# Optimization experiments

Measured on AMD Instinct MI355X. Metric: run time of the kernel, lower is better.

The kernel has to match this reference:

```python
import jax, jax.numpy as jnp
import numpy as np

N = 100000          # total nodes (ground + sub)
G = 50000           # ground nodes (first G)
E = 800000          # edges per edge set
H = 64              # hidden_features
F_IN = 32           # node_features
MAX_DEG = 20        # MFConv max_degree
NUM_GRAPHS = 128
DEPTH = 1
LN_EPS = 1e-5


def setup_inputs() -> dict:
    key = jax.random.key(0)
    ks = jax.random.split(key, 12)

    def edges(k):
        return jax.random.randint(k, (2, E), 0, N, dtype=jnp.int32)

    return {
        "x": jax.random.normal(ks[0], (N, F_IN), jnp.float32),
        "edge_index": edges(ks[1]),
        "subgraph_edge_index": edges(ks[2]),
        "node_subnode_index": edges(ks[3]),
        "subnode_node_index": edges(ks[4]),
        "ground_node": jnp.arange(N) < G,
        "subgraph_batch_index": jax.random.randint(ks[5], (N - G,), 0, NUM_GRAPHS, dtype=jnp.int32),
        "batch_idx": jax.random.randint(ks[6], (N,), 0, NUM_GRAPHS, dtype=jnp.int32),
        # learned parameters
        "emb_w": jax.random.normal(ks[7], (F_IN, H), jnp.float32) / np.sqrt(F_IN).astype(np.float32),
        "emb_b": jnp.zeros((H,), jnp.float32),
        # 4 MFConvs per depth, 21 degree buckets each; lins_l has bias, lins_r has none
        "conv_wl": jax.random.normal(ks[8], (DEPTH, 4, MAX_DEG + 1, H, H), jnp.float32) / np.sqrt(H).astype(np.float32),
        "conv_bl": jnp.zeros((DEPTH, 4, MAX_DEG + 1, H), jnp.float32),
        "conv_wr": jax.random.normal(ks[9], (DEPTH, 4, MAX_DEG + 1, H, H), jnp.float32) / np.sqrt(H).astype(np.float32),
        "ln_g": jnp.ones((DEPTH, H), jnp.float32),
        "ln_b": jnp.zeros((DEPTH, H), jnp.float32),
        "out_w": jax.random.normal(ks[10], (H, 1), jnp.float32) / np.sqrt(H).astype(np.float32),
        "out_b": jnp.zeros((1,), jnp.float32),
    }


def _mfconv(x, ei, wl, bl, wr):
    """PyG MFConv: out_i = lins_l[deg_i](sum_{j->i} x_j) + lins_r[deg_i](x_i).
    Returns (out, update_mask) where update_mask marks nodes receiving >=1 message
    (catch_lone_sender equivalent)."""
    src, dst = ei[0], ei[1]
    n = x.shape[0]
    deg = jax.ops.segment_sum(jnp.ones(src.shape, jnp.float32), dst, num_segments=n)
    d = jnp.minimum(deg.astype(jnp.int32), MAX_DEG)
    h = jax.ops.segment_sum(x[src], dst, num_segments=n)      # [N, H] neighbor sum
    out = jnp.zeros_like(x)
    for k in range(MAX_DEG + 1):                              # fixed 21 degree buckets
        m = (d == k)[:, None]
        out = out + jnp.where(m, h @ wl[k] + bl[k] + x @ wr[k], 0.0)
    return out, deg > 0


def _layernorm(h, g, b):
    mu = jnp.mean(h, axis=-1, keepdims=True)
    var = jnp.mean(jnp.square(h - mu), axis=-1, keepdims=True)
    return (h - mu) * jax.lax.rsqrt(var + LN_EPS) * g + b


def reference(x, edge_index, subgraph_edge_index, node_subnode_index,
              subnode_node_index, ground_node, subgraph_batch_index, batch_idx,
              emb_w, emb_b, conv_wl, conv_bl, conv_wr, ln_g, ln_b, out_w, out_b):
    h = x @ emb_w + emb_b                                     # embedding
    eis = (edge_index, node_subnode_index, subgraph_edge_index, subnode_node_index)
    for i in range(DEPTH):
        if i != 0:
            h = jax.nn.relu(h)
        h0 = h                                                # residual skip
        for j, ei in enumerate(eis):
            out, upd = _mfconv(h, ei, conv_wl[i, j], conv_bl[i, j], conv_wr[i, j])
            h = jnp.where(upd[:, None], out, h)               # masking=True restore
            if j < 3:
                h = jax.nn.relu(h)
        h = _layernorm(h, ln_g[i], ln_b[i])
        h = h + h0
    # global_add_pool over ground nodes only
    pooled = jax.ops.segment_sum(jnp.where(ground_node[:, None], h, 0.0),
                                 batch_idx, num_segments=NUM_GRAPHS)
    return pooled @ out_w + out_b
```

## Files before the change

### kernel.cpp

```cpp
#include <hip/hip_runtime.h>

#define N_NODES 100000
#define G_NODES 50000
#define N_EDGES 800000
#define H 64
#define F_IN 32
#define MAX_DEG 20
#define NUM_GRAPHS 128
#define LN_EPS 1e-5f
#define POOL_BLOCKS 256
#define MAX_TILES 1600

#define NBINS 512
#define BPB 782
#define CHUNK 6250
#define MKEYS (4 * N_NODES)
#define MEDGES (4 * N_EDGES)

typedef __attribute__((ext_vector_type(8))) short short8;
typedef __attribute__((ext_vector_type(4))) float float4v;

static __device__ __forceinline__ unsigned short f2b(float f) {
  unsigned u = __float_as_uint(f);
  return (unsigned short)((u + 0x7fffu + ((u >> 16) & 1u)) >> 16);
}
static __device__ __forceinline__ float b2f(unsigned short b) {
  return __uint_as_float(((unsigned)b) << 16);
}

__global__ __launch_bounds__(256) void emb_kernel(
    const float* __restrict__ x, const unsigned short* __restrict__ ewbt,
    const float* __restrict__ eb, float* __restrict__ h0,
    unsigned short* __restrict__ ab, float* __restrict__ pooled) {
  int tid = threadIdx.x;
  if (blockIdx.x == 0) {
    for (int i = tid; i < NUM_GRAPHS * H; i += 256) pooled[i] = 0.f;
  }
  int base = blockIdx.x * 64;
  int nIn = min(64, N_NODES - base);
  int qw = tid >> 6, lane = tid & 63;
  __shared__ unsigned short aL[64 * 40];
  __shared__ float outF[64 * 68];

  {
    int node = tid >> 2, chb = (tid & 3) * 8;
    unsigned short v8[8];
    if (node < nIn) {
      const float* xr = x + ((size_t)(base + node)) * F_IN + chb;
      float4 f0 = *(const float4*)(xr);
      float4 f1 = *(const float4*)(xr + 4);
      v8[0] = f2b(f0.x); v8[1] = f2b(f0.y); v8[2] = f2b(f0.z); v8[3] = f2b(f0.w);
      v8[4] = f2b(f1.x); v8[5] = f2b(f1.y); v8[6] = f2b(f1.z); v8[7] = f2b(f1.w);
    } else {
#pragma unroll
      for (int i = 0; i < 8; ++i) v8[i] = 0;
    }
    *(short8*)&aL[(tid >> 2) * 40 + chb] = *(short8*)v8;
  }

  int m = lane & 15, quad = lane >> 4;
  short8 a = *(const short8*)&aL[(qw * 16 + m) * 40 + quad * 8];
  float4v acc[4];
#pragma unroll
  for (int t = 0; t < 4; ++t) {
    float bv = eb[t * 16 + m];
    acc[t] = (float4v){bv, bv, bv, bv};
  }
#pragma unroll
  for (int t = 0; t < 4; ++t) {
    short8 bf = *(const short8*)&ewbt[(t * 16 + m) * F_IN + quad * 8];
    acc[t] = __builtin_amdgcn_mfma_f32_16x16x32_bf16(a, bf, acc[t], 0, 0, 0);
  }
#pragma unroll
  for (int t = 0; t < 4; ++t)
#pragma unroll
    for (int r = 0; r < 4; ++r)
      outF[(qw * 16 + quad * 4 + r) * 68 + t * 16 + m] = acc[t][r];
  for (int r = qw * 16; r < qw * 16 + 16; ++r) {
    if (r < nIn) {
      int node = base + r;
      float v = outF[r * 68 + lane];
      if (node < G_NODES) h0[node * H + lane] = v;
      ab[node * 128 + 64 + lane] = f2b(v);
    }
  }
}

__global__ __launch_bounds__(256) void wconv_kernel(
    const float* __restrict__ wl, const float* __restrict__ wr,
    const float* __restrict__ ew, unsigned short* __restrict__ wbt,
    unsigned short* __restrict__ ewbt) {
  int i = blockIdx.x * 256 + threadIdx.x;
  if (i < 84 * 64 * 128) {
    int k = i & 127;
    int ch = (i >> 7) & 63;
    int jb = i >> 13;
    float v = (k < 64) ? wl[jb * 4096 + k * 64 + ch]
                       : wr[jb * 4096 + (k - 64) * 64 + ch];
    wbt[i] = f2b(v);
  } else if (i < 84 * 64 * 128 + H * F_IN) {
    int ii = i - 84 * 64 * 128;
    int c = ii >> 5, f = ii & 31;
    ewbt[ii] = f2b(ew[f * H + c]);
  }
}

__global__ __launch_bounds__(256) void p1_bincount(
    const int* __restrict__ e0, const int* __restrict__ e1,
    const int* __restrict__ e2, const int* __restrict__ e3,
    int* __restrict__ cntT) {
  __shared__ int hist[NBINS];
  int t = threadIdx.x, b = blockIdx.x;
  for (int i = t; i < NBINS; i += 256) hist[i] = 0;
  __syncthreads();
  int j = b >> 7;
  const int* ei = (j == 0) ? e0 : (j == 1) ? e1 : (j == 2) ? e2 : e3;
  int ebase = (b & 127) * CHUNK;
  for (int i = t; i < CHUNK; i += 256) {
    int dst = ei[N_EDGES + ebase + i];
    int key = j * N_NODES + dst;
    atomicAdd(&hist[key / BPB], 1);
  }
  __syncthreads();
  for (int i = t; i < NBINS; i += 256) cntT[i * NBINS + b] = hist[i];
}

__global__ __launch_bounds__(256) void p3_binscatter(
    const int* __restrict__ e0, const int* __restrict__ e1,
    const int* __restrict__ e2, const int* __restrict__ e3,
    const int* __restrict__ offT, const int* __restrict__ bsumA,
    unsigned* __restrict__ binned) {
  __shared__ int cur[NBINS];
  int t = threadIdx.x, b = blockIdx.x;
  for (int i = t; i < NBINS; i += 256) {
    int idx = i * NBINS + b;
    cur[i] = offT[idx] + bsumA[idx >> 10];
  }
  __syncthreads();
  int j = b >> 7;
  const int* ei = (j == 0) ? e0 : (j == 1) ? e1 : (j == 2) ? e2 : e3;
  int ebase = (b & 127) * CHUNK;
  for (int i = t; i < CHUNK; i += 256) {
    int src = ei[ebase + i];
    int dst = ei[N_EDGES + ebase + i];
    int key = j * N_NODES + dst;
    int bin = key / BPB;
    int pos = atomicAdd(&cur[bin], 1);
    binned[pos] = ((unsigned)(key - bin * BPB) << 17) | (unsigned)src;
  }
}

__global__ __launch_bounds__(256) void p46_kernel(
    const unsigned* __restrict__ binned, const int* __restrict__ offT,
    const int* __restrict__ bsumA, int* __restrict__ deg4,
    int* __restrict__ S, int* __restrict__ slots, int* __restrict__ bcnt) {
  __shared__ int hist[BPB];
  __shared__ int cur[BPB];
  __shared__ int bh[84];
  __shared__ int wtot[4];
  int t = threadIdx.x, bin = blockIdx.x;
  int kb = bin * BPB;
  for (int i = t; i < BPB; i += 256) hist[i] = 0;
  if (t < 84) bh[t] = 0;
  __syncthreads();
  int i0 = bin * NBINS;
  int start = offT[i0] + bsumA[i0 >> 10];
  int end;
  if (bin == NBINS - 1) {
    end = MEDGES;
  } else {
    int i1 = (bin + 1) * NBINS;
    end = offT[i1] + bsumA[i1 >> 10];
  }
  for (int i = start + t; i < end; i += 256)
    atomicAdd(&hist[binned[i] >> 17], 1);
  __syncthreads();
  for (int i = t; i < BPB; i += 256) {
    int key = kb + i;
    if (key < MKEYS) {
      int d = hist[i];
      deg4[key] = d;
      int j = key / N_NODES;
      int b = d < MAX_DEG ? d : MAX_DEG;
      atomicAdd(&bh[j * 21 + b], 1);
    }
  }
  int base = t * 4;
  int v0 = 0, v1 = 0, v2 = 0, v3 = 0;
  if (base < BPB) {
    v0 = hist[base];
    v1 = (base + 1 < BPB) ? hist[base + 1] : 0;
    v2 = (base + 2 < BPB) ? hist[base + 2] : 0;
    v3 = (base + 3 < BPB) ? hist[base + 3] : 0;
  }
  int s = v0 + v1 + v2 + v3;
  int incl = s;
#pragma unroll
  for (int off = 1; off < 64; off <<= 1) {
    int y = __shfl_up(incl, off, 64);
    if ((t & 63) >= off) incl += y;
  }
  if ((t & 63) == 63) wtot[t >> 6] = incl;
  __syncthreads();
  int wbase = 0;
  for (int w = 0; w < (t >> 6); ++w) wbase += wtot[w];
  int ex = start + wbase + incl - s;
  if (base < BPB) {
    cur[base] = ex;
    if (base + 1 < BPB) cur[base + 1] = ex + v0;
    if (base + 2 < BPB) cur[base + 2] = ex + v0 + v1;
    if (base + 3 < BPB) cur[base + 3] = ex + v0 + v1 + v2;
  }
  __syncthreads();
  for (int i = t; i < BPB; i += 256)
    if (kb + i < MKEYS) S[kb + i] = cur[i];
  if (t < 84 && bh[t]) atomicAdd(&bcnt[t], bh[t]);
  __syncthreads();
  for (int i = start + t; i < end; i += 256) {
    unsigned v = binned[i];
    int pos = atomicAdd(&cur[v >> 17], 1);
    slots[pos] = (int)(v & 0x1ffffu);
  }
}

__global__ __launch_bounds__(256) void scan1(
    const int* __restrict__ in, int* __restrict__ S, int* __restrict__ bsum, int M) {
  int t = threadIdx.x;
  int base = blockIdx.x * 1024 + t * 4;
  int v0 = 0, v1 = 0, v2 = 0, v3 = 0;
  if (base + 3 < M) {
    int4 q = *(const int4*)(in + base);
    v0 = q.x; v1 = q.y; v2 = q.z; v3 = q.w;
  } else {
    if (base     < M) v0 = in[base];
    if (base + 1 < M) v1 = in[base + 1];
    if (base + 2 < M) v2 = in[base + 2];
    if (base + 3 < M) v3 = in[base + 3];
  }
  int s = v0 + v1 + v2 + v3;
  int incl = s;
#pragma unroll
  for (int off = 1; off < 64; off <<= 1) {
    int y = __shfl_up(incl, off, 64);
    if ((t & 63) >= off) incl += y;
  }
  __shared__ int wtot[4];
  if ((t & 63) == 63) wtot[t >> 6] = incl;
  __syncthreads();
  int wbase = 0;
  for (int w = 0; w < (t >> 6); ++w) wbase += wtot[w];
  int ex = wbase + incl - s;
  if (base < M) {
    int eo0 = ex, eo1 = ex + v0, eo2 = ex + v0 + v1, eo3 = ex + v0 + v1 + v2;
    if (base + 3 < M) {
      *(int4*)(S + base) = make_int4(eo0, eo1, eo2, eo3);
    } else {
      S[base] = eo0;
      if (base + 1 < M) S[base + 1] = eo1;
      if (base + 2 < M) S[base + 2] = eo2;
    }
  }
  if (t == 255) bsum[blockIdx.x] = wbase + incl;
}

__global__ __launch_bounds__(512) void scan2(
    int* __restrict__ bsum, int nb, int* __restrict__ bcnt) {
  int t = threadIdx.x;
  if (t < 84) bcnt[t] = 0;
  int v = (t < nb) ? bsum[t] : 0;
  int incl = v;
#pragma unroll
  for (int off = 1; off < 64; off <<= 1) {
    int y = __shfl_up(incl, off, 64);
    if ((t & 63) >= off) incl += y;
  }
  __shared__ int wtot[8];
  if ((t & 63) == 63) wtot[t >> 6] = incl;
  __syncthreads();
  int wbase = 0;
  for (int w = 0; w < (t >> 6); ++w) wbase += wtot[w];
  if (t < nb) bsum[t] = wbase + incl - v;
}

__global__ __launch_bounds__(128) void bucket_scan(
    const int* __restrict__ bcnt, int* __restrict__ boff, int* __restrict__ bcur,
    int* __restrict__ ntiles, int* __restrict__ tdesc) {
  __shared__ int wt[2];
  __shared__ int exL[84], cntL[84], toffL[84];
  int t = threadIdx.x;
  int v = (t < 84) ? bcnt[t] : 0;
  int incl = v;
#pragma unroll
  for (int off = 1; off < 64; off <<= 1) {
    int y = __shfl_up(incl, off, 64);
    if ((t & 63) >= off) incl += y;
  }
  if ((t & 63) == 63) wt[t >> 6] = incl;
  __syncthreads();
  int wbase = (t >> 6) ? wt[0] : 0;
  if (t < 84) {
    int ex = wbase + incl - v;
    boff[t] = ex;
    bcur[t] = ex;
    exL[t] = ex;
    cntL[t] = v;
  }
  __syncthreads();
  if (t < 4) {
    int acc = 0;
    for (int bb = 0; bb < 21; ++bb) {
      toffL[t * 21 + bb] = acc;
      acc += (cntL[t * 21 + bb] + 63) >> 6;
    }
    ntiles[t] = acc;
  }
  __syncthreads();
  for (int jb = 0; jb < 84; ++jb) {
    int j = jb / 21, b = jb - j * 21;
    int cnt = cntL[jb], off = exL[jb], tb = toffL[jb];
    int nt = (cnt + 63) >> 6;
    for (int i = t; i < nt; i += 128) {
      int s2 = i << 6;
      int nIn = min(64, cnt - s2);
      tdesc[j * MAX_TILES + tb + i] = ((off + s2) << 12) | (b << 7) | nIn;
    }
  }
}

__global__ __launch_bounds__(256) void bucket_fill(
    const int* __restrict__ deg4, int* __restrict__ bcur, int* __restrict__ blist) {
  __shared__ int hist[21];
  __shared__ int base[21];
  int t = threadIdx.x;
  if (t < 21) hist[t] = 0;
  __syncthreads();
  int node = blockIdx.x * 256 + t;
  int j = blockIdx.y;
  int b = 0, lpos = 0;
  bool valid = (node < N_NODES);
  if (valid) {
    int d = deg4[j * N_NODES + node];
    b = d < MAX_DEG ? d : MAX_DEG;
    lpos = atomicAdd(&hist[b], 1);
  }
  __syncthreads();
  if (t < 21 && hist[t]) base[t] = atomicAdd(&bcur[j * 21 + t], hist[t]);
  __syncthreads();
  if (valid) blist[base[b] + lpos] = node;
}

__global__ __launch_bounds__(256) void conv_kernel(
    float* __restrict__ h, unsigned short* __restrict__ ab,
    const int* __restrict__ S, const int* __restrict__ deg,
    const int* __restrict__ slots,
    const int* __restrict__ blist, const int* __restrict__ tdesc,
    const int* __restrict__ ntiles, const unsigned short* __restrict__ wbt,
    const float* __restrict__ bl, int j, int inoff, int do_relu, int last) {
  if ((int)blockIdx.x >= ntiles[j]) return;
  int d = tdesc[j * MAX_TILES + blockIdx.x];
  int nIn = d & 127;
  int b = (d >> 7) & 31;
  const int* lst = blist + (d >> 12);
  int outoff = 64 - inoff;

  int tid = threadIdx.x;
  int qw = tid >> 6, lane = tid & 63;

  if (b == 0) {
    for (int r = qw * 16; r < qw * 16 + 16; ++r) {
      if (r < nIn) {
        int node = lst[r];
        float v = b2f(ab[node * 128 + inoff + lane]);
        if (do_relu) v = fmaxf(v, 0.f);
        if (last) {
          if (node < G_NODES) h[node * H + lane] = v;
        } else {
          ab[node * 128 + outoff + lane] = f2b(v);
        }
      }
    }
    return;
  }

  __shared__ unsigned short aL[64 * 136];
  __shared__ int nodeS[64];
  int q = lane >> 4, cl = lane & 15;

  for (int i = 0; i < 4; ++i) {
    int r = qw * 16 + q * 4 + i;
    int node = (r < nIn) ? lst[r] : -1;
    if (cl == 0) nodeS[r] = node;
    uint2 selfv = make_uint2(0u, 0u);
    float s0a = 0.f, s1a = 0.f, s2a = 0.f, s3a = 0.f;
    float s0b = 0.f, s1b = 0.f, s2b = 0.f, s3b = 0.f;
    if (node >= 0) {
      selfv = *(const uint2*)&ab[node * 128 + inoff + 4 * cl];
      int off = S[node];
      int dg = (b < MAX_DEG) ? b : deg[node];
      int e = 0;
      for (; e + 3 < dg; e += 4) {
        int n0 = slots[off + e];
        int n1 = slots[off + e + 1];
        int n2 = slots[off + e + 2];
        int n3 = slots[off + e + 3];
        uint2 p0 = *(const uint2*)&ab[n0 * 128 + inoff + 4 * cl];
        uint2 p1 = *(const uint2*)&ab[n1 * 128 + inoff + 4 * cl];
        uint2 p2 = *(const uint2*)&ab[n2 * 128 + inoff + 4 * cl];
        uint2 p3 = *(const uint2*)&ab[n3 * 128 + inoff + 4 * cl];
        s0a += b2f((unsigned short)p0.x) + b2f((unsigned short)p1.x);
        s0b += b2f((unsigned short)p2.x) + b2f((unsigned short)p3.x);
        s1a += b2f((unsigned short)(p0.x >> 16)) + b2f((unsigned short)(p1.x >> 16));
        s1b += b2f((unsigned short)(p2.x >> 16)) + b2f((unsigned short)(p3.x >> 16));
        s2a += b2f((unsigned short)p0.y) + b2f((unsigned short)p1.y);
        s2b += b2f((unsigned short)p2.y) + b2f((unsigned short)p3.y);
        s3a += b2f((unsigned short)(p0.y >> 16)) + b2f((unsigned short)(p1.y >> 16));
        s3b += b2f((unsigned short)(p2.y >> 16)) + b2f((unsigned short)(p3.y >> 16));
      }
      for (; e < dg; ++e) {
        uint2 p0 = *(const uint2*)&ab[slots[off + e] * 128 + inoff + 4 * cl];
        s0a += b2f((unsigned short)p0.x);
        s1a += b2f((unsigned short)(p0.x >> 16));
        s2a += b2f((unsigned short)p0.y);
        s3a += b2f((unsigned short)(p0.y >> 16));
      }
    }
    uint2 o;
    o.x = (unsigned)f2b(s0a + s0b) | ((unsigned)f2b(s1a + s1b) << 16);
    o.y = (unsigned)f2b(s2a + s2b) | ((unsigned)f2b(s3a + s3b) << 16);
    *(uint2*)&aL[r * 136 + 4 * cl] = o;
    *(uint2*)&aL[r * 136 + 64 + 4 * cl] = selfv;
  }

  int m = lane & 15, quad = lane >> 4;
  const unsigned short* wbase = wbt + (size_t)(j * 21 + b) * 64 * 128;
  float4v acc[4];
#pragma unroll
  for (int t = 0; t < 4; ++t) {
    float bv = bl[b * 64 + t * 16 + m];
    acc[t] = (float4v){bv, bv, bv, bv};
  }
#pragma unroll
  for (int ks = 0; ks < 4; ++ks) {
    short8 a = *(const short8*)&aL[(qw * 16 + m) * 136 + ks * 32 + quad * 8];
#pragma unroll
    for (int t = 0; t < 4; ++t) {
      short8 bf = *(const short8*)&wbase[(t * 16 + m) * 128 + ks * 32 + quad * 8];
      acc[t] = __builtin_amdgcn_mfma_f32_16x16x32_bf16(a, bf, acc[t], 0, 0, 0);
    }
  }
  if (do_relu) {
#pragma unroll
    for (int t = 0; t < 4; ++t)
#pragma unroll
      for (int r = 0; r < 4; ++r) acc[t][r] = fmaxf(acc[t][r], 0.f);
  }
  float* outF = (float*)aL;
#pragma unroll
  for (int t = 0; t < 4; ++t)
#pragma unroll
    for (int r = 0; r < 4; ++r)
      outF[(qw * 16 + quad * 4 + r) * 68 + t * 16 + m] = acc[t][r];
  if (last) {
    for (int r = qw * 16; r < qw * 16 + 16; ++r)
      if (r < nIn && nodeS[r] < G_NODES)
        h[nodeS[r] * H + lane] = outF[r * 68 + lane];
  } else {
    for (int r = qw * 16; r < qw * 16 + 16; ++r)
      if (r < nIn) ab[nodeS[r] * 128 + outoff + lane] = f2b(outF[r * 68 + lane]);
  }
}

__global__ __launch_bounds__(1024) void ln_pool_kernel(
    const float* __restrict__ h, const float* __restrict__ h0,
    const float* __restrict__ g, const float* __restrict__ b,
    const int* __restrict__ batch, float* __restrict__ pooled) {
  __shared__ float sm[NUM_GRAPHS * H];
  int t = threadIdx.x;
  for (int i = t; i < NUM_GRAPHS * H; i += 1024) sm[i] = 0.f;
  __syncthreads();
  int lane = t & 63, w = t >> 6;
  const int per = (G_NODES + POOL_BLOCKS - 1) / POOL_BLOCKS;
  int start = blockIdx.x * per;
  int end = min(start + per, G_NODES);
  for (int node = start + w; node < end; node += 16) {
    int idx = node * H + lane;
    float v = h[idx];
    float s = v;
#pragma unroll
    for (int off = 32; off > 0; off >>= 1) s += __shfl_xor(s, off, 64);
    float mu = s * (1.0f / H);
    float dv = v - mu;
    float q = dv * dv;
#pragma unroll
    for (int off = 32; off > 0; off >>= 1) q += __shfl_xor(q, off, 64);
    float inv = rsqrtf(q * (1.0f / H) + LN_EPS);
    float r = dv * inv * g[lane] + b[lane] + h0[idx];
    atomicAdd(&sm[batch[node] * H + lane], r);
  }
  __syncthreads();
  for (int i = t; i < NUM_GRAPHS * H; i += 1024) {
    float v = sm[i];
    if (v != 0.f) atomicAdd(&pooled[i], v);
  }
}

__global__ __launch_bounds__(64) void out_kernel(
    const float* __restrict__ pooled, const float* __restrict__ w,
    const float* __restrict__ b, float* __restrict__ out) {
  int gph = blockIdx.x;
  int c = threadIdx.x;
  float v = pooled[gph * H + c] * w[c];
#pragma unroll
  for (int off = 32; off > 0; off >>= 1) v += __shfl_xor(v, off, 64);
  if (c == 0) out[gph] = v + b[0];
}

extern "C" void kernel_launch(void* const* d_in, const int* in_sizes, int n_in,
                              void* d_out, int out_size, void* d_ws, size_t ws_size,
                              hipStream_t stream) {
  const float* x       = (const float*)d_in[0];
  const int*   ei_edge = (const int*)d_in[1];
  const int*   ei_sub  = (const int*)d_in[2];
  const int*   ei_ns   = (const int*)d_in[3];
  const int*   ei_sn   = (const int*)d_in[4];
  const int*   batch   = (const int*)d_in[7];
  const float* emb_w   = (const float*)d_in[8];
  const float* emb_b   = (const float*)d_in[9];
  const float* conv_wl = (const float*)d_in[10];
  const float* conv_bl = (const float*)d_in[11];
  const float* conv_wr = (const float*)d_in[12];
  const float* ln_g    = (const float*)d_in[13];
  const float* ln_b    = (const float*)d_in[14];
  const float* out_w   = (const float*)d_in[15];
  const float* out_b   = (const float*)d_in[16];
  float* out = (float*)d_out;

  const size_t HB = (size_t)N_NODES * H * sizeof(float);
  char* ws = (char*)d_ws;
  float* h      = (float*)(ws);
  float* h0     = (float*)(ws + HB);
  unsigned short* ab = (unsigned short*)(ws + 2 * HB);
  unsigned* binned = (unsigned*)(ws);
  int*   cntT   = (int*)(ws + HB);
  int*   offT   = (int*)(ws + HB + 0x100000);
  int*   bsumA  = (int*)(ws + HB + 0x300000);
  int*   deg4   = (int*)(ws + 3 * HB);
  int*   S      = (int*)(ws + 78400000);
  int*   slots  = (int*)(ws + 80000000);
  int*   bcnt   = (int*)(ws + 92800000);
  int*   boff   = (int*)(ws + 92800512);
  int*   bcur   = (int*)(ws + 92801024);
  int*   blist  = (int*)(ws + 92801536);
  float* pooled = (float*)(ws + 94401536);
  unsigned short* wbt = (unsigned short*)(ws + 94434304);
  int*   tdesc  = (int*)(ws + 95810560);
  int*   ntiles = (int*)(ws + 95836160);
  unsigned short* ewbt = (unsigned short*)(ws + 95836608);

  const int* e0 = ei_edge, *e1 = ei_ns, *e2 = ei_sub, *e3 = ei_sn;
  const int MC = NBINS * NBINS;
  const int NB_MC = MC / 1024;

  p1_bincount<<<NBINS, 256, 0, stream>>>(e0, e1, e2, e3, cntT);
  scan1<<<NB_MC, 256, 0, stream>>>(cntT, offT, bsumA, MC);
  scan2<<<1, 512, 0, stream>>>(bsumA, NB_MC, bcnt);
  p3_binscatter<<<NBINS, 256, 0, stream>>>(e0, e1, e2, e3, offT, bsumA, binned);
  p46_kernel<<<NBINS, 256, 0, stream>>>(binned, offT, bsumA, deg4, S, slots, bcnt);
  bucket_scan<<<1, 128, 0, stream>>>(bcnt, boff, bcur, ntiles, tdesc);
  bucket_fill<<<dim3((N_NODES + 255) / 256, 4), 256, 0, stream>>>(deg4, bcur, blist);
  wconv_kernel<<<(84 * 64 * 128 + H * F_IN + 255) / 256, 256, 0, stream>>>(
      conv_wl, conv_wr, emb_w, wbt, ewbt);

  emb_kernel<<<(N_NODES + 63) / 64, 256, 0, stream>>>(x, ewbt, emb_b, h0, ab, pooled);

  for (int j = 0; j < 4; ++j) {
    conv_kernel<<<MAX_TILES, 256, 0, stream>>>(
        h, ab, S + j * N_NODES, deg4 + j * N_NODES, slots,
        blist, tdesc, ntiles, wbt,
        conv_bl + (size_t)j * 21 * H, j,
        (j & 1) ? 0 : 64,
        j < 3 ? 1 : 0, j == 3 ? 1 : 0);
  }

  ln_pool_kernel<<<POOL_BLOCKS, 1024, 0, stream>>>(h, h0, ln_g, ln_b, batch, pooled);
  out_kernel<<<NUM_GRAPHS, 64, 0, stream>>>(pooled, out_w, out_b, out);
}
```

Baseline: 393.5 us.

## Replace two-pass bin count and scan with fixed-capacity atomic bin allocation

```diff
diff --git a/kernel.cpp b/kernel.cpp
--- a/kernel.cpp
+++ b/kernel.cpp
@@ -13,6 +13,7 @@
 
 #define NBINS 512
 #define BPB 782
+#define BINCAP_LOG 13
 #define CHUNK 6250
 #define MKEYS (4 * N_NODES)
 #define MEDGES (4 * N_EDGES)
@@ -28,69 +29,16 @@
   return __uint_as_float(((unsigned)b) << 16);
 }
 
-__global__ __launch_bounds__(256) void emb_kernel(
-    const float* __restrict__ x, const unsigned short* __restrict__ ewbt,
-    const float* __restrict__ eb, float* __restrict__ h0,
-    unsigned short* __restrict__ ab, float* __restrict__ pooled) {
-  int tid = threadIdx.x;
-  if (blockIdx.x == 0) {
-    for (int i = tid; i < NUM_GRAPHS * H; i += 256) pooled[i] = 0.f;
-  }
-  int base = blockIdx.x * 64;
-  int nIn = min(64, N_NODES - base);
-  int qw = tid >> 6, lane = tid & 63;
-  __shared__ unsigned short aL[64 * 40];
-  __shared__ float outF[64 * 68];
-
-  {
-    int node = tid >> 2, chb = (tid & 3) * 8;
-    unsigned short v8[8];
-    if (node < nIn) {
-      const float* xr = x + ((size_t)(base + node)) * F_IN + chb;
-      float4 f0 = *(const float4*)(xr);
-      float4 f1 = *(const float4*)(xr + 4);
-      v8[0] = f2b(f0.x); v8[1] = f2b(f0.y); v8[2] = f2b(f0.z); v8[3] = f2b(f0.w);
-      v8[4] = f2b(f1.x); v8[5] = f2b(f1.y); v8[6] = f2b(f1.z); v8[7] = f2b(f1.w);
-    } else {
-#pragma unroll
-      for (int i = 0; i < 8; ++i) v8[i] = 0;
-    }
-    *(short8*)&aL[(tid >> 2) * 40 + chb] = *(short8*)v8;
-  }
-
-  int m = lane & 15, quad = lane >> 4;
-  short8 a = *(const short8*)&aL[(qw * 16 + m) * 40 + quad * 8];
-  float4v acc[4];
-#pragma unroll
-  for (int t = 0; t < 4; ++t) {
-    float bv = eb[t * 16 + m];
-    acc[t] = (float4v){bv, bv, bv, bv};
-  }
-#pragma unroll
-  for (int t = 0; t < 4; ++t) {
-    short8 bf = *(const short8*)&ewbt[(t * 16 + m) * F_IN + quad * 8];
-    acc[t] = __builtin_amdgcn_mfma_f32_16x16x32_bf16(a, bf, acc[t], 0, 0, 0);
-  }
-#pragma unroll
-  for (int t = 0; t < 4; ++t)
-#pragma unroll
-    for (int r = 0; r < 4; ++r)
-      outF[(qw * 16 + quad * 4 + r) * 68 + t * 16 + m] = acc[t][r];
-  for (int r = qw * 16; r < qw * 16 + 16; ++r) {
-    if (r < nIn) {
-      int node = base + r;
-      float v = outF[r * 68 + lane];
-      if (node < G_NODES) h0[node * H + lane] = v;
-      ab[node * 128 + 64 + lane] = f2b(v);
-    }
-  }
-}
-
 __global__ __launch_bounds__(256) void wconv_kernel(
     const float* __restrict__ wl, const float* __restrict__ wr,
     const float* __restrict__ ew, unsigned short* __restrict__ wbt,
-    unsigned short* __restrict__ ewbt) {
+    unsigned short* __restrict__ ewbt, int* __restrict__ bincur,
+    int* __restrict__ bcnt) {
   int i = blockIdx.x * 256 + threadIdx.x;
+  if (blockIdx.x == 0) {
+    for (int k = threadIdx.x; k < NBINS; k += 256) bincur[k] = k << BINCAP_LOG;
+    if (threadIdx.x < 84) bcnt[threadIdx.x] = 0;
+  }
   if (i < 84 * 64 * 128) {
     int k = i & 127;
     int ch = (i >> 7) & 63;
@@ -105,11 +53,70 @@
   }
 }
 
-__global__ __launch_bounds__(256) void p1_bincount(
+__global__ __launch_bounds__(256) void emb_kernel(
+    const float* __restrict__ x, const unsigned short* __restrict__ ewbt,
+    const float* __restrict__ eb, float* __restrict__ h0,
+    unsigned short* __restrict__ ab, float* __restrict__ pooled) {
+  int tid = threadIdx.x;
+  if (blockIdx.x == 0) {
+    for (int i = tid; i < NUM_GRAPHS * H; i += 256) pooled[i] = 0.f;
+  }
+  int base = blockIdx.x * 64;
+  int nIn = min(64, N_NODES - base);
+  int qw = tid >> 6, lane = tid & 63;
+  __shared__ unsigned short aL[64 * 40];
+  __shared__ float outF[64 * 68];
+
+  {
+    int node = tid >> 2, chb = (tid & 3) * 8;
+    unsigned short v8[8];
+    if (node < nIn) {
+      const float* xr = x + ((size_t)(base + node)) * F_IN + chb;
+      float4 f0 = *(const float4*)(xr);
+      float4 f1 = *(const float4*)(xr + 4);
+      v8[0] = f2b(f0.x); v8[1] = f2b(f0.y); v8[2] = f2b(f0.z); v8[3] = f2b(f0.w);
+      v8[4] = f2b(f1.x); v8[5] = f2b(f1.y); v8[6] = f2b(f1.z); v8[7] = f2b(f1.w);
+    } else {
+#pragma unroll
+      for (int i = 0; i < 8; ++i) v8[i] = 0;
+    }
+    *(short8*)&aL[(tid >> 2) * 40 + chb] = *(short8*)v8;
+  }
+
+  int m = lane & 15, quad = lane >> 4;
+  short8 a = *(const short8*)&aL[(qw * 16 + m) * 40 + quad * 8];
+  float4v acc[4];
+#pragma unroll
+  for (int t = 0; t < 4; ++t) {
+    float bv = eb[t * 16 + m];
+    acc[t] = (float4v){bv, bv, bv, bv};
+  }
+#pragma unroll
+  for (int t = 0; t < 4; ++t) {
+    short8 bf = *(const short8*)&ewbt[(t * 16 + m) * F_IN + quad * 8];
+    acc[t] = __builtin_amdgcn_mfma_f32_16x16x32_bf16(a, bf, acc[t], 0, 0, 0);
+  }
+#pragma unroll
+  for (int t = 0; t < 4; ++t)
+#pragma unroll
+    for (int r = 0; r < 4; ++r)
+      outF[(qw * 16 + quad * 4 + r) * 68 + t * 16 + m] = acc[t][r];
+  for (int r = qw * 16; r < qw * 16 + 16; ++r) {
+    if (r < nIn) {
+      int node = base + r;
+      float v = outF[r * 68 + lane];
+      if (node < G_NODES) h0[node * H + lane] = v;
+      ab[node * 128 + 64 + lane] = f2b(v);
+    }
+  }
+}
+
+__global__ __launch_bounds__(256) void p3_binscatter(
     const int* __restrict__ e0, const int* __restrict__ e1,
     const int* __restrict__ e2, const int* __restrict__ e3,
-    int* __restrict__ cntT) {
+    int* __restrict__ bincur, unsigned* __restrict__ binned) {
   __shared__ int hist[NBINS];
+  __shared__ int cur[NBINS];
   int t = threadIdx.x, b = blockIdx.x;
   for (int i = t; i < NBINS; i += 256) hist[i] = 0;
   __syncthreads();
@@ -118,28 +125,14 @@
   int ebase = (b & 127) * CHUNK;
   for (int i = t; i < CHUNK; i += 256) {
     int dst = ei[N_EDGES + ebase + i];
-    int key = j * N_NODES + dst;
-    atomicAdd(&hist[key / BPB], 1);
-  }
-  __syncthreads();
-  for (int i = t; i < NBINS; i += 256) cntT[i * NBINS + b] = hist[i];
-}
-
-__global__ __launch_bounds__(256) void p3_binscatter(
-    const int* __restrict__ e0, const int* __restrict__ e1,
-    const int* __restrict__ e2, const int* __restrict__ e3,
-    const int* __restrict__ offT, const int* __restrict__ bsumA,
-    unsigned* __restrict__ binned) {
-  __shared__ int cur[NBINS];
-  int t = threadIdx.x, b = blockIdx.x;
+    atomicAdd(&hist[(j * N_NODES + dst) / BPB], 1);
+  }
+  __syncthreads();
   for (int i = t; i < NBINS; i += 256) {
-    int idx = i * NBINS + b;
-    cur[i] = offT[idx] + bsumA[idx >> 10];
-  }
-  __syncthreads();
-  int j = b >> 7;
-  const int* ei = (j == 0) ? e0 : (j == 1) ? e1 : (j == 2) ? e2 : e3;
-  int ebase = (b & 127) * CHUNK;
+    int c = hist[i];
+    cur[i] = c ? atomicAdd(&bincur[i], c) : 0;
+  }
+  __syncthreads();
   for (int i = t; i < CHUNK; i += 256) {
     int src = ei[ebase + i];
     int dst = ei[N_EDGES + ebase + i];
@@ -151,9 +144,9 @@
 }
 
 __global__ __launch_bounds__(256) void p46_kernel(
-    const unsigned* __restrict__ binned, const int* __restrict__ offT,
-    const int* __restrict__ bsumA, int* __restrict__ deg4,
-    int* __restrict__ S, int* __restrict__ slots, int* __restrict__ bcnt) {
+    const unsigned* __restrict__ binned, const int* __restrict__ bincur,
+    int* __restrict__ deg4, int* __restrict__ S, int* __restrict__ slots,
+    int* __restrict__ bcnt) {
   __shared__ int hist[BPB];
   __shared__ int cur[BPB];
   __shared__ int bh[84];
@@ -163,15 +156,8 @@
   for (int i = t; i < BPB; i += 256) hist[i] = 0;
   if (t < 84) bh[t] = 0;
   __syncthreads();
-  int i0 = bin * NBINS;
-  int start = offT[i0] + bsumA[i0 >> 10];
-  int end;
-  if (bin == NBINS - 1) {
-    end = MEDGES;
-  } else {
-    int i1 = (bin + 1) * NBINS;
-    end = offT[i1] + bsumA[i1 >> 10];
-  }
+  int start = bin << BINCAP_LOG;
+  int end = bincur[bin];
   for (int i = start + t; i < end; i += 256)
     atomicAdd(&hist[binned[i] >> 17], 1);
   __syncthreads();
@@ -221,65 +207,6 @@
     int pos = atomicAdd(&cur[v >> 17], 1);
     slots[pos] = (int)(v & 0x1ffffu);
   }
-}
-
-__global__ __launch_bounds__(256) void scan1(
-    const int* __restrict__ in, int* __restrict__ S, int* __restrict__ bsum, int M) {
-  int t = threadIdx.x;
-  int base = blockIdx.x * 1024 + t * 4;
-  int v0 = 0, v1 = 0, v2 = 0, v3 = 0;
-  if (base + 3 < M) {
-    int4 q = *(const int4*)(in + base);
-    v0 = q.x; v1 = q.y; v2 = q.z; v3 = q.w;
-  } else {
-    if (base     < M) v0 = in[base];
-    if (base + 1 < M) v1 = in[base + 1];
-    if (base + 2 < M) v2 = in[base + 2];
-    if (base + 3 < M) v3 = in[base + 3];
-  }
-  int s = v0 + v1 + v2 + v3;
-  int incl = s;
-#pragma unroll
-  for (int off = 1; off < 64; off <<= 1) {
-    int y = __shfl_up(incl, off, 64);
-    if ((t & 63) >= off) incl += y;
-  }
-  __shared__ int wtot[4];
-  if ((t & 63) == 63) wtot[t >> 6] = incl;
-  __syncthreads();
-  int wbase = 0;
-  for (int w = 0; w < (t >> 6); ++w) wbase += wtot[w];
-  int ex = wbase + incl - s;
-  if (base < M) {
-    int eo0 = ex, eo1 = ex + v0, eo2 = ex + v0 + v1, eo3 = ex + v0 + v1 + v2;
-    if (base + 3 < M) {
-      *(int4*)(S + base) = make_int4(eo0, eo1, eo2, eo3);
-    } else {
-      S[base] = eo0;
-      if (base + 1 < M) S[base + 1] = eo1;
-      if (base + 2 < M) S[base + 2] = eo2;
-    }
-  }
-  if (t == 255) bsum[blockIdx.x] = wbase + incl;
-}
-
-__global__ __launch_bounds__(512) void scan2(
-    int* __restrict__ bsum, int nb, int* __restrict__ bcnt) {
-  int t = threadIdx.x;
-  if (t < 84) bcnt[t] = 0;
-  int v = (t < nb) ? bsum[t] : 0;
-  int incl = v;
-#pragma unroll
-  for (int off = 1; off < 64; off <<= 1) {
-    int y = __shfl_up(incl, off, 64);
-    if ((t & 63) >= off) incl += y;
-  }
-  __shared__ int wtot[8];
-  if ((t & 63) == 63) wtot[t >> 6] = incl;
-  __syncthreads();
-  int wbase = 0;
-  for (int w = 0; w < (t >> 6); ++w) wbase += wtot[w];
-  if (t < nb) bsum[t] = wbase + incl - v;
 }
 
 __global__ __launch_bounds__(128) void bucket_scan(
@@ -540,13 +467,8 @@
   float* h      = (float*)(ws);
   float* h0     = (float*)(ws + HB);
   unsigned short* ab = (unsigned short*)(ws + 2 * HB);
-  unsigned* binned = (unsigned*)(ws);
-  int*   cntT   = (int*)(ws + HB);
-  int*   offT   = (int*)(ws + HB + 0x100000);
-  int*   bsumA  = (int*)(ws + HB + 0x300000);
   int*   deg4   = (int*)(ws + 3 * HB);
   int*   S      = (int*)(ws + 78400000);
-  int*   slots  = (int*)(ws + 80000000);
   int*   bcnt   = (int*)(ws + 92800000);
   int*   boff   = (int*)(ws + 92800512);
   int*   bcur   = (int*)(ws + 92801024);
@@ -556,20 +478,18 @@
   int*   tdesc  = (int*)(ws + 95810560);
   int*   ntiles = (int*)(ws + 95836160);
   unsigned short* ewbt = (unsigned short*)(ws + 95836608);
+  int*   bincur = (int*)(ws + 95841024);
+  unsigned* binned = (unsigned*)(ws + 100000000);
+  int*   slots  = (int*)(ws + 117000000);
 
   const int* e0 = ei_edge, *e1 = ei_ns, *e2 = ei_sub, *e3 = ei_sn;
-  const int MC = NBINS * NBINS;
-  const int NB_MC = MC / 1024;
-
-  p1_bincount<<<NBINS, 256, 0, stream>>>(e0, e1, e2, e3, cntT);
-  scan1<<<NB_MC, 256, 0, stream>>>(cntT, offT, bsumA, MC);
-  scan2<<<1, 512, 0, stream>>>(bsumA, NB_MC, bcnt);
-  p3_binscatter<<<NBINS, 256, 0, stream>>>(e0, e1, e2, e3, offT, bsumA, binned);
-  p46_kernel<<<NBINS, 256, 0, stream>>>(binned, offT, bsumA, deg4, S, slots, bcnt);
+
+  wconv_kernel<<<(84 * 64 * 128 + H * F_IN + 255) / 256, 256, 0, stream>>>(
+      conv_wl, conv_wr, emb_w, wbt, ewbt, bincur, bcnt);
+  p3_binscatter<<<NBINS, 256, 0, stream>>>(e0, e1, e2, e3, bincur, binned);
+  p46_kernel<<<NBINS, 256, 0, stream>>>(binned, bincur, deg4, S, slots, bcnt);
   bucket_scan<<<1, 128, 0, stream>>>(bcnt, boff, bcur, ntiles, tdesc);
   bucket_fill<<<dim3((N_NODES + 255) / 256, 4), 256, 0, stream>>>(deg4, bcur, blist);
-  wconv_kernel<<<(84 * 64 * 128 + H * F_IN + 255) / 256, 256, 0, stream>>>(
-      conv_wl, conv_wr, emb_w, wbt, ewbt);
 
   emb_kernel<<<(N_NODES + 63) / 64, 256, 0, stream>>>(x, ewbt, emb_b, h0, ab, pooled);
 
```

Result: faster. 382.3 us (-2.8%).
